# Performance work log

Measured on AMD Instinct MI355X. Metric: run time of the kernel, lower is better.

The kernel has to match this reference:

```python
import jax, jax.numpy as jnp
import numpy as np

N_NODES = 50000
N_EDGES = 800000
N_GRAPHS = 128


def gcn_conv(x, row, col, W, b, num_nodes):
    # GCNConv: x' = D^-1/2 (A + I) D^-1/2 (x W) + b, with self-loops added.
    h = x @ W  # [N, out]
    # append self-loops
    sl = jnp.arange(num_nodes, dtype=row.dtype)
    r = jnp.concatenate([row, sl])
    c = jnp.concatenate([col, sl])
    deg = jax.ops.segment_sum(jnp.ones_like(r, dtype=h.dtype), r, num_segments=num_nodes)
    dinv = jnp.where(deg > 0, jax.lax.rsqrt(deg), 0.0)
    norm = dinv[r] * dinv[c]  # [E+N]
    msg = h[c] * norm[:, None]  # gather + scale
    out = jax.ops.segment_sum(msg, r, num_segments=num_nodes)
    return out + b


def setup_inputs() -> dict:
    key = jax.random.key(0)
    k = jax.random.split(key, 6)
    x = jax.random.normal(k[0], (N_NODES, 256), dtype=jnp.float32)
    edge_index = jax.random.randint(k[1], (2, N_EDGES), 0, N_NODES, dtype=jnp.int32)
    batch = jnp.sort(jax.random.randint(k[2], (N_NODES,), 0, N_GRAPHS, dtype=jnp.int32))
    W1 = jax.random.normal(k[3], (256, 128), dtype=jnp.float32) * (1.0 / np.sqrt(256))
    b1 = jnp.zeros((128,), dtype=jnp.float32)
    W2 = jax.random.normal(k[4], (128, 32), dtype=jnp.float32) * (1.0 / np.sqrt(128))
    b2 = jnp.zeros((32,), dtype=jnp.float32)
    return {"x": x, "edge_index": edge_index, "batch": batch,
            "W1": W1, "b1": b1, "W2": W2, "b2": b2}


def reference(x, edge_index, batch, W1, b1, W2, b2):
    row, col = edge_index[0], edge_index[1]
    h = gcn_conv(x, row, col, W1, b1, N_NODES)
    h = jax.nn.relu(h)
    # dropout is identity in eval mode (training=False)
    h = gcn_conv(h, row, col, W2, b2, N_NODES)
    # global_mean_pool over batch ids
    sums = jax.ops.segment_sum(h, batch, num_segments=N_GRAPHS)
    cnts = jax.ops.segment_sum(jnp.ones((N_NODES,), dtype=h.dtype), batch, num_segments=N_GRAPHS)
    pooled = sums / jnp.clip(cnts, 1.0)[:, None]  # [G, num_classes]
    return jax.nn.log_softmax(pooled, axis=1)
```

## Files before the change

### kernel.cpp

```cpp
#include <hip/hip_runtime.h>
#include <math.h>

#define N_NODES 50000
#define N_EDGES 800000
#define N_GRAPHS 128
#define DIM0 256
#define DIM1 128
#define DIM2 32

#define NBUCK 196
#define NEB 98

using f32x4 = __attribute__((ext_vector_type(4))) float;
using s16x8 = __attribute__((ext_vector_type(8))) short;

__device__ inline unsigned bf16pack(float a, float b) {
    unsigned ua = __float_as_uint(a), ub = __float_as_uint(b);
    ua = (ua + 0x7fffu + ((ua >> 16) & 1u)) >> 16;
    ub = (ub + 0x7fffu + ((ub >> 16) & 1u)) >> 16;
    return ua | (ub << 16);
}
__device__ inline float2 bf16x2(unsigned p) {
    return make_float2(__uint_as_float(p << 16), __uint_as_float(p & 0xffff0000u));
}

__device__ inline int featOf(int p) {
    return 32 * (p >> 5) + ((p >> 1) & 15) + 16 * (p & 1);
}

__global__ __launch_bounds__(256) void k_hist(const int* __restrict__ row, int* __restrict__ hist) {
    __shared__ int h[NBUCK];
    int b = blockIdx.x, t = threadIdx.x;
    if (t < NBUCK) h[t] = 0;
    __syncthreads();
#pragma unroll
    for (int i = 0; i < 8; ++i) {
        int idx = b * 2048 + i * 256 + t;
        if (idx < N_EDGES / 4) {
            int4 r4 = ((const int4*)row)[idx];
            atomicAdd(&h[r4.x >> 8], 1);
            atomicAdd(&h[r4.y >> 8], 1);
            atomicAdd(&h[r4.z >> 8], 1);
            atomicAdd(&h[r4.w >> 8], 1);
        }
    }
    __syncthreads();
    if (t < NBUCK) hist[b * NBUCK + t] = h[t];
}

__global__ __launch_bounds__(256) void k_place(const int* __restrict__ row, const int* __restrict__ col,
                                               const int* __restrict__ hist, uint* __restrict__ bb,
                                               int* __restrict__ bbase, int* __restrict__ btot,
                                               const float* __restrict__ W1, uint* __restrict__ W1b,
                                               const float* __restrict__ W2, uint* __restrict__ W2b,
                                               const int* __restrict__ batch, int* gstart,
                                               float* __restrict__ pooled) {
    __shared__ int cur[NBUCK];
    __shared__ int tot[NBUCK];
    __shared__ int sc[256];
    int blk = blockIdx.x, t = threadIdx.x;
    if (blk >= NEB) {
        if (blk == NEB + 16) {
            for (int i = t; i < N_GRAPHS * DIM2; i += 256) pooled[i] = 0.f;
            return;
        }
        int g = (blk - NEB) * 256 + t;
        {
            int s = g >> 9, tt = (g >> 6) & 7, q = (g >> 4) & 3, n = g & 15;
            int k0 = s * 32 + q * 8;
            int colw = tt * 16 + n;
            uint4 o;
            o.x = bf16pack(W1[(size_t)(k0 + 0) * DIM1 + colw], W1[(size_t)(k0 + 1) * DIM1 + colw]);
            o.y = bf16pack(W1[(size_t)(k0 + 2) * DIM1 + colw], W1[(size_t)(k0 + 3) * DIM1 + colw]);
            o.z = bf16pack(W1[(size_t)(k0 + 4) * DIM1 + colw], W1[(size_t)(k0 + 5) * DIM1 + colw]);
            o.w = bf16pack(W1[(size_t)(k0 + 6) * DIM1 + colw], W1[(size_t)(k0 + 7) * DIM1 + colw]);
            ((uint4*)W1b)[g] = o;
        }
        if (g < 512) {
            int s = g >> 7, tt = (g >> 6) & 1, l = g & 63;
            int n = tt * 16 + (l & 15);
            int kb = s * 32 + (l >> 4) * 8;
            uint4 o;
            o.x = bf16pack(W2[(size_t)featOf(kb + 0) * DIM2 + n], W2[(size_t)featOf(kb + 1) * DIM2 + n]);
            o.y = bf16pack(W2[(size_t)featOf(kb + 2) * DIM2 + n], W2[(size_t)featOf(kb + 3) * DIM2 + n]);
            o.z = bf16pack(W2[(size_t)featOf(kb + 4) * DIM2 + n], W2[(size_t)featOf(kb + 5) * DIM2 + n]);
            o.w = bf16pack(W2[(size_t)featOf(kb + 6) * DIM2 + n], W2[(size_t)featOf(kb + 7) * DIM2 + n]);
            ((uint4*)W2b)[g] = o;
        }
        if (g <= N_GRAPHS) {
            int lo = 0, hi = N_NODES;
            while (lo < hi) { int mid = (lo + hi) >> 1; if (batch[mid] < g) lo = mid + 1; else hi = mid; }
            gstart[g] = lo;
        }
        return;
    }
    int pre = 0, to = 0;
    for (int b2 = 0; b2 < NEB; ++b2) {
        int v = (t < NBUCK) ? hist[b2 * NBUCK + t] : 0;
        to += v;
        if (b2 < blk) pre += v;
    }
    if (t < NBUCK) tot[t] = to;
    sc[t] = (t < NBUCK) ? to : 0;
    __syncthreads();
    for (int off = 1; off < 256; off <<= 1) {
        int x = (t >= off) ? sc[t - off] : 0;
        __syncthreads();
        sc[t] += x;
        __syncthreads();
    }
    if (t < NBUCK) {
        int base = sc[t] - tot[t];
        cur[t] = base + pre;
        if (blk == 0) { bbase[t] = base; btot[t] = tot[t]; }
    }
    __syncthreads();
#pragma unroll
    for (int i = 0; i < 8; ++i) {
        int idx = blk * 2048 + i * 256 + t;
        if (idx < N_EDGES / 4) {
            int4 r4 = ((const int4*)row)[idx];
            int4 c4 = ((const int4*)col)[idx];
            int rs[4] = {r4.x, r4.y, r4.z, r4.w};
            int cs[4] = {c4.x, c4.y, c4.z, c4.w};
#pragma unroll
            for (int j = 0; j < 4; ++j) {
                int pos = atomicAdd(&cur[rs[j] >> 8], 1);
                bb[pos] = ((uint)(rs[j] & 255) << 16) | (uint)cs[j];
            }
        }
    }
}

__global__ __launch_bounds__(256) void k_build(const int* __restrict__ bbase, const int* __restrict__ btot,
                                               const uint* __restrict__ bb,
                                               int* __restrict__ offs, int* __restrict__ cnt,
                                               ushort* __restrict__ csr) {
    __shared__ int c256[256];
    __shared__ int cur256[256];
    __shared__ int wsum[4];
    int b = blockIdx.x, t = threadIdx.x;
    int start = bbase[b];
    int n = btot[b];
    c256[t] = 0;
    __syncthreads();
    for (int i = t; i < n; i += 256) atomicAdd(&c256[bb[start + i] >> 16], 1);
    __syncthreads();
    int w = t >> 6, l = t & 63;
    int v = c256[t];
    int incl = v;
#pragma unroll
    for (int off = 1; off < 64; off <<= 1) {
        int x = __shfl_up(incl, off, 64);
        if (l >= off) incl += x;
    }
    if (l == 63) wsum[w] = incl;
    __syncthreads();
    int woff = 0;
    for (int i = 0; i < w; ++i) woff += wsum[i];
    int excl = incl - v + woff;
    cur256[t] = excl;
    int r = b * 256 + t;
    if (r < N_NODES) { offs[r] = start + excl; cnt[r] = v; }
    __syncthreads();
    for (int i = t; i < n; i += 256) {
        uint e = bb[start + i];
        int pos = atomicAdd(&cur256[e >> 16], 1);
        csr[start + pos] = (ushort)(e & 0xFFFFu);
    }
}

#define G1_BM 128
#define AS_LD 20
__global__ __launch_bounds__(256) void k_gemm1(const float* __restrict__ X, const uint* __restrict__ W1b,
                                               const int* __restrict__ cnt, unsigned* __restrict__ h1u) {
    __shared__ uint w1s[16384];
    __shared__ uint As[G1_BM * AS_LD];
    int t = threadIdx.x;
    int w = t >> 6, lane = t & 63, q = lane >> 4, m16 = lane & 15;
    int rowBase = blockIdx.x * G1_BM;

    {
        const uint4* src = (const uint4*)W1b;
        uint4* dst = (uint4*)w1s;
#pragma unroll
        for (int i = 0; i < 16; ++i) dst[i * 256 + t] = src[i * 256 + t];
    }

    f32x4 acc[2][8];
#pragma unroll
    for (int i = 0; i < 2; ++i)
#pragma unroll
        for (int j = 0; j < 8; ++j) acc[i][j] = (f32x4){0.f, 0.f, 0.f, 0.f};

    int ar = t >> 1, ah = t & 1;
    for (int s = 0; s < 8; ++s) {
        float4 f0 = {0,0,0,0}, f1 = {0,0,0,0}, f2 = {0,0,0,0}, f3 = {0,0,0,0};
        int grow = rowBase + ar;
        if (grow < N_NODES) {
            const float* src = X + (size_t)grow * DIM0 + s * 32 + ah * 16;
            f0 = *(const float4*)(src + 0);
            f1 = *(const float4*)(src + 4);
            f2 = *(const float4*)(src + 8);
            f3 = *(const float4*)(src + 12);
        }
        uint4 p0, p1;
        p0.x = bf16pack(f0.x, f0.y); p0.y = bf16pack(f0.z, f0.w);
        p0.z = bf16pack(f1.x, f1.y); p0.w = bf16pack(f1.z, f1.w);
        p1.x = bf16pack(f2.x, f2.y); p1.y = bf16pack(f2.z, f2.w);
        p1.z = bf16pack(f3.x, f3.y); p1.w = bf16pack(f3.z, f3.w);
        __syncthreads();
        *(uint4*)&As[ar * AS_LD + ah * 8 + 0] = p0;
        *(uint4*)&As[ar * AS_LD + ah * 8 + 4] = p1;
        __syncthreads();

        s16x8 af[2];
#pragma unroll
        for (int rt = 0; rt < 2; ++rt) {
            int arow = w * 32 + rt * 16 + m16;
            af[rt] = *(s16x8*)&As[arow * AS_LD + q * 4];
        }
#pragma unroll
        for (int tt = 0; tt < 8; ++tt) {
            s16x8 bf = *(s16x8*)&w1s[((s * 8 + tt) * 64 + lane) * 4];
            acc[0][tt] = __builtin_amdgcn_mfma_f32_16x16x32_bf16(af[0], bf, acc[0][tt], 0, 0, 0);
            acc[1][tt] = __builtin_amdgcn_mfma_f32_16x16x32_bf16(af[1], bf, acc[1][tt], 0, 0, 0);
        }
    }

#pragma unroll
    for (int rt = 0; rt < 2; ++rt) {
#pragma unroll
        for (int reg = 0; reg < 4; ++reg) {
            int row = rowBase + w * 32 + rt * 16 + q * 4 + reg;
            if (row < N_NODES) {
                float dv = rsqrtf((float)(cnt[row] + 1));
                unsigned* hr = h1u + (size_t)row * 64;
#pragma unroll
                for (int u = 0; u < 4; ++u)
                    hr[u * 16 + m16] = bf16pack(acc[rt][2 * u][reg] * dv, acc[rt][2 * u + 1][reg] * dv);
            }
        }
    }
}

#define A1_LD 68
__global__ __launch_bounds__(256) void k_agg1g2(const unsigned* __restrict__ h1u, const int* __restrict__ cnt,
                                                const int* __restrict__ offs, const ushort* __restrict__ csr,
                                                const float* __restrict__ b1, const uint* __restrict__ W2b,
                                                unsigned* __restrict__ h2u) {
    __shared__ uint a1tile[16 * A1_LD];
    __shared__ float sdi[16];
    int t = threadIdx.x;
    int wv = t >> 6, lane = t & 63;
    int nb16 = blockIdx.x * 16;

#pragma unroll
    for (int i = 0; i < 4; ++i) {
        int m = wv * 4 + i;
        int node = nb16 + m;
        float2 acc = bf16x2(h1u[(size_t)node * 64 + lane]);
        int n = cnt[node];
        const ushort* cp = csr + offs[node];
        int ec = 0;
        if (lane < n) ec = cp[lane];
        int j = 0;
        for (; j + 8 <= n; j += 8) {
            int c0 = __shfl(ec, j),     c1 = __shfl(ec, j + 1), c2 = __shfl(ec, j + 2), c3 = __shfl(ec, j + 3);
            int c4 = __shfl(ec, j + 4), c5 = __shfl(ec, j + 5), c6 = __shfl(ec, j + 6), c7 = __shfl(ec, j + 7);
            unsigned p0 = h1u[(size_t)c0 * 64 + lane];
            unsigned p1 = h1u[(size_t)c1 * 64 + lane];
            unsigned p2 = h1u[(size_t)c2 * 64 + lane];
            unsigned p3 = h1u[(size_t)c3 * 64 + lane];
            unsigned p4 = h1u[(size_t)c4 * 64 + lane];
            unsigned p5 = h1u[(size_t)c5 * 64 + lane];
            unsigned p6 = h1u[(size_t)c6 * 64 + lane];
            unsigned p7 = h1u[(size_t)c7 * 64 + lane];
            float2 v0 = bf16x2(p0), v1 = bf16x2(p1), v2 = bf16x2(p2), v3 = bf16x2(p3);
            float2 v4 = bf16x2(p4), v5 = bf16x2(p5), v6 = bf16x2(p6), v7 = bf16x2(p7);
            acc.x += (v0.x + v1.x) + (v2.x + v3.x) + (v4.x + v5.x) + (v6.x + v7.x);
            acc.y += (v0.y + v1.y) + (v2.y + v3.y) + (v4.y + v5.y) + (v6.y + v7.y);
        }
        for (; j + 4 <= n; j += 4) {
            int c0 = __shfl(ec, j), c1 = __shfl(ec, j + 1), c2 = __shfl(ec, j + 2), c3 = __shfl(ec, j + 3);
            unsigned p0 = h1u[(size_t)c0 * 64 + lane];
            unsigned p1 = h1u[(size_t)c1 * 64 + lane];
            unsigned p2 = h1u[(size_t)c2 * 64 + lane];
            unsigned p3 = h1u[(size_t)c3 * 64 + lane];
            float2 v0 = bf16x2(p0), v1 = bf16x2(p1), v2 = bf16x2(p2), v3 = bf16x2(p3);
            acc.x += (v0.x + v1.x) + (v2.x + v3.x);
            acc.y += (v0.y + v1.y) + (v2.y + v3.y);
        }
        for (; j < n; ++j) {
            int c = __shfl(ec, j);
            float2 v = bf16x2(h1u[(size_t)c * 64 + lane]);
            acc.x += v.x; acc.y += v.y;
        }
        float di = rsqrtf((float)(n + 1));
        if (lane == 0) sdi[m] = di;
        int f0 = (lane >> 4) * 32 + (lane & 15);
        acc.x = fmaxf(acc.x * di + b1[f0], 0.f);
        acc.y = fmaxf(acc.y * di + b1[f0 + 16], 0.f);
        a1tile[m * A1_LD + lane] = bf16pack(acc.x, acc.y);
    }
    __syncthreads();

    if (wv == 0) {
        int q = lane >> 4, m16 = lane & 15;
        f32x4 accA = (f32x4){0.f, 0.f, 0.f, 0.f};
        f32x4 accB = (f32x4){0.f, 0.f, 0.f, 0.f};
#pragma unroll
        for (int s = 0; s < 4; ++s) {
            s16x8 af = *(s16x8*)&a1tile[m16 * A1_LD + s * 16 + q * 4];
            s16x8 bf0 = *(const s16x8*)(W2b + (size_t)((s * 2 + 0) * 64 + lane) * 4);
            s16x8 bf1 = *(const s16x8*)(W2b + (size_t)((s * 2 + 1) * 64 + lane) * 4);
            accA = __builtin_amdgcn_mfma_f32_16x16x32_bf16(af, bf0, accA, 0, 0, 0);
            accB = __builtin_amdgcn_mfma_f32_16x16x32_bf16(af, bf1, accB, 0, 0, 0);
        }
#pragma unroll
        for (int r = 0; r < 4; ++r) {
            int node = nb16 + q * 4 + r;
            float dv = sdi[q * 4 + r];
            h2u[(size_t)node * 16 + m16] = bf16pack(accA[r] * dv, accB[r] * dv);
        }
    }
}

__global__ __launch_bounds__(256) void k_agg2pool(const unsigned* __restrict__ h2u, const int* __restrict__ cnt,
                                                  const int* __restrict__ offs, const ushort* __restrict__ csr,
                                                  const int* __restrict__ batch, float* __restrict__ pooled) {
    __shared__ float2 red[16][16];
    int t = threadIdx.x;
    int nb16 = blockIdx.x * 16;
    int node = nb16 + (t >> 4);
    int l = t & 15;
    float2 acc = bf16x2(h2u[(size_t)node * 16 + l]);
    int n = cnt[node];
    const ushort* cp = csr + offs[node];
    for (int base = 0; base < n; base += 16) {
        int m = min(16, n - base);
        int ec = 0;
        if (l < m) ec = cp[base + l];
        int j = 0;
        for (; j + 4 <= m; j += 4) {
            int c0 = __shfl(ec, j, 16), c1 = __shfl(ec, j + 1, 16);
            int c2 = __shfl(ec, j + 2, 16), c3 = __shfl(ec, j + 3, 16);
            unsigned p0 = h2u[(size_t)c0 * 16 + l];
            unsigned p1 = h2u[(size_t)c1 * 16 + l];
            unsigned p2 = h2u[(size_t)c2 * 16 + l];
            unsigned p3 = h2u[(size_t)c3 * 16 + l];
            float2 v0 = bf16x2(p0), v1 = bf16x2(p1), v2 = bf16x2(p2), v3 = bf16x2(p3);
            acc.x += v0.x + v1.x + v2.x + v3.x;
            acc.y += v0.y + v1.y + v2.y + v3.y;
        }
        for (; j < m; ++j) {
            int c = __shfl(ec, j, 16);
            float2 v = bf16x2(h2u[(size_t)c * 16 + l]);
            acc.x += v.x; acc.y += v.y;
        }
    }
    float di = rsqrtf((float)(n + 1));
    red[t >> 4][l] = make_float2(acc.x * di, acc.y * di);
    __syncthreads();
    if (t < 16) {
        float2 run = make_float2(0.f, 0.f);
        int gprev = batch[nb16];
        for (int m = 0; m < 16; ++m) {
            int g = batch[nb16 + m];
            if (g != gprev) {
                atomicAdd(&pooled[gprev * DIM2 + t], run.x);
                atomicAdd(&pooled[gprev * DIM2 + t + 16], run.y);
                run = make_float2(0.f, 0.f);
                gprev = g;
            }
            float2 v = red[m][t];
            run.x += v.x; run.y += v.y;
        }
        atomicAdd(&pooled[gprev * DIM2 + t], run.x);
        atomicAdd(&pooled[gprev * DIM2 + t + 16], run.y);
    }
}

__global__ __launch_bounds__(64) void k_final(const float* __restrict__ pooled, const int* __restrict__ gstart,
                                              const float* __restrict__ b2, float* __restrict__ out) {
    int g = blockIdx.x;
    int lane = threadIdx.x;
    float cntf = fmaxf((float)(gstart[g + 1] - gstart[g]), 1.0f);
    float val = 0.f, v = -INFINITY;
    if (lane < DIM2) {
        val = pooled[g * DIM2 + lane] / cntf + b2[lane];
        v = val;
    }
#pragma unroll
    for (int m = 16; m >= 1; m >>= 1) v = fmaxf(v, __shfl_xor(v, m, 32));
    float ex = (lane < DIM2) ? expf(val - v) : 0.f;
#pragma unroll
    for (int m = 16; m >= 1; m >>= 1) ex += __shfl_xor(ex, m, 32);
    if (lane < DIM2) out[g * DIM2 + lane] = val - v - logf(ex);
}

extern "C" void kernel_launch(void* const* d_in, const int* in_sizes, int n_in,
                              void* d_out, int out_size, void* d_ws, size_t ws_size,
                              hipStream_t stream) {
    const float* x     = (const float*)d_in[0];
    const int*   eidx  = (const int*)d_in[1];
    const int*   batch = (const int*)d_in[2];
    const float* W1    = (const float*)d_in[3];
    const float* b1    = (const float*)d_in[4];
    const float* W2    = (const float*)d_in[5];
    const float* b2    = (const float*)d_in[6];
    const int* row = eidx;
    const int* col = eidx + N_EDGES;
    float* out = (float*)d_out;

    char* p = (char*)d_ws;
    int*    cnt    = (int*)p;    p += (size_t)N_NODES * 4;
    int*    offs   = (int*)p;    p += (size_t)N_NODES * 4 + 16;
    int*    gstart = (int*)p;    p += 768;
    uint*   W1b    = (uint*)p;   p += 4096 * 16;
    uint*   W2b    = (uint*)p;   p += 512 * 16;
    int*    hist   = (int*)p;    p += (size_t)NEB * NBUCK * 4 + 32;
    int*    bbase  = (int*)p;    p += 1024;
    int*    btot   = (int*)p;    p += 1024;
    float*  pooled = (float*)p;  p += (size_t)N_GRAPHS * DIM2 * 4;
    uint*   bb     = (uint*)p;   p += (size_t)N_EDGES * 4;
    ushort* csr    = (ushort*)p; p += (size_t)N_EDGES * 2;
    unsigned* h1u  = (unsigned*)p; p += (size_t)N_NODES * 64 * 4;
    unsigned* h2u  = (unsigned*)p; p += (size_t)N_NODES * 16 * 4;

    k_hist<<<NEB, 256, 0, stream>>>(row, hist);
    k_place<<<NEB + 17, 256, 0, stream>>>(row, col, hist, bb, bbase, btot,
                                          W1, W1b, W2, W2b, batch, gstart, pooled);
    k_build<<<NBUCK, 256, 0, stream>>>(bbase, btot, bb, offs, cnt, csr);

    k_gemm1<<<(N_NODES + G1_BM - 1) / G1_BM, 256, 0, stream>>>(x, W1b, cnt, h1u);
    k_agg1g2<<<N_NODES / 16, 256, 0, stream>>>(h1u, cnt, offs, csr, b1, W2b, h2u);
    k_agg2pool<<<N_NODES / 16, 256, 0, stream>>>(h2u, cnt, offs, csr, batch, pooled);
    k_final<<<N_GRAPHS, 64, 0, stream>>>(pooled, gstart, b2, out);
}
```

Measured before the change: 191.5 us.

## Fuse CSR construction into one cooperative kernel with global-atomic counting sort

Replaces the three-kernel bucketed CSR build (histogram, bucket placement, per-bucket build) with a single cooperative kernel. It counts per-node degrees with global atomics, runs a grid-wide prefix scan across grid.sync barriers, then scatters column indices with global atomic cursors. This removes two launches and the intermediate bucket buffer. In exchange it relies on contended global atomics on 50k counters, adds five grid-wide barriers, and no longer orders edges deterministically within a row.

```diff
diff --git a/kernel.cpp b/kernel.cpp
--- a/kernel.cpp
+++ b/kernel.cpp
@@ -1,5 +1,8 @@
 #include <hip/hip_runtime.h>
+#include <hip/hip_cooperative_groups.h>
 #include <math.h>
+
+namespace cg = cooperative_groups;
 
 #define N_NODES 50000
 #define N_EDGES 800000
@@ -8,8 +11,7 @@
 #define DIM1 128
 #define DIM2 32
 
-#define NBUCK 196
-#define NEB 98
+#define PRE_GRID 196
 
 using f32x4 = __attribute__((ext_vector_type(4))) float;
 using s16x8 = __attribute__((ext_vector_type(8))) short;
@@ -28,55 +30,46 @@
     return 32 * (p >> 5) + ((p >> 1) & 15) + 16 * (p & 1);
 }
 
-__global__ __launch_bounds__(256) void k_hist(const int* __restrict__ row, int* __restrict__ hist) {
-    __shared__ int h[NBUCK];
+__global__ __launch_bounds__(256) void k_pre(
+    const int* __restrict__ row, const int* __restrict__ col,
+    const float* __restrict__ W1, uint* __restrict__ W1b,
+    const float* __restrict__ W2, uint* __restrict__ W2b,
+    const int* __restrict__ batch, int* __restrict__ gstart,
+    float* __restrict__ pooled,
+    int* __restrict__ deg, int* __restrict__ offs, int* __restrict__ cur,
+    ushort* __restrict__ csr, int* __restrict__ blockTot)
+{
+    cg::grid_group grid = cg::this_grid();
+    __shared__ int wsum[4];
+    __shared__ int sc[256];
     int b = blockIdx.x, t = threadIdx.x;
-    if (t < NBUCK) h[t] = 0;
-    __syncthreads();
-#pragma unroll
-    for (int i = 0; i < 8; ++i) {
-        int idx = b * 2048 + i * 256 + t;
-        if (idx < N_EDGES / 4) {
-            int4 r4 = ((const int4*)row)[idx];
-            atomicAdd(&h[r4.x >> 8], 1);
-            atomicAdd(&h[r4.y >> 8], 1);
-            atomicAdd(&h[r4.z >> 8], 1);
-            atomicAdd(&h[r4.w >> 8], 1);
-        }
-    }
-    __syncthreads();
-    if (t < NBUCK) hist[b * NBUCK + t] = h[t];
-}
-
-__global__ __launch_bounds__(256) void k_place(const int* __restrict__ row, const int* __restrict__ col,
-                                               const int* __restrict__ hist, uint* __restrict__ bb,
-                                               int* __restrict__ bbase, int* __restrict__ btot,
-                                               const float* __restrict__ W1, uint* __restrict__ W1b,
-                                               const float* __restrict__ W2, uint* __restrict__ W2b,
-                                               const int* __restrict__ batch, int* gstart,
-                                               float* __restrict__ pooled) {
-    __shared__ int cur[NBUCK];
-    __shared__ int tot[NBUCK];
-    __shared__ int sc[256];
-    int blk = blockIdx.x, t = threadIdx.x;
-    if (blk >= NEB) {
-        if (blk == NEB + 16) {
-            for (int i = t; i < N_GRAPHS * DIM2; i += 256) pooled[i] = 0.f;
-            return;
-        }
-        int g = (blk - NEB) * 256 + t;
-        {
-            int s = g >> 9, tt = (g >> 6) & 7, q = (g >> 4) & 3, n = g & 15;
-            int k0 = s * 32 + q * 8;
-            int colw = tt * 16 + n;
-            uint4 o;
-            o.x = bf16pack(W1[(size_t)(k0 + 0) * DIM1 + colw], W1[(size_t)(k0 + 1) * DIM1 + colw]);
-            o.y = bf16pack(W1[(size_t)(k0 + 2) * DIM1 + colw], W1[(size_t)(k0 + 3) * DIM1 + colw]);
-            o.z = bf16pack(W1[(size_t)(k0 + 4) * DIM1 + colw], W1[(size_t)(k0 + 5) * DIM1 + colw]);
-            o.w = bf16pack(W1[(size_t)(k0 + 6) * DIM1 + colw], W1[(size_t)(k0 + 7) * DIM1 + colw]);
-            ((uint4*)W1b)[g] = o;
-        }
-        if (g < 512) {
+    int idx = b * 256 + t;
+
+    if (idx < N_NODES) deg[idx] = 0;
+    if (b < 16) pooled[idx] = 0.f;
+    grid.sync();
+
+    const int nI4 = N_EDGES / 4;
+    for (int i = idx; i < nI4; i += PRE_GRID * 256) {
+        int4 r4 = ((const int4*)row)[i];
+        atomicAdd(&deg[r4.x], 1);
+        atomicAdd(&deg[r4.y], 1);
+        atomicAdd(&deg[r4.z], 1);
+        atomicAdd(&deg[r4.w], 1);
+    }
+    if (b < 16) {
+        int g = idx;
+        int s = g >> 9, tt = (g >> 6) & 7, q = (g >> 4) & 3, n = g & 15;
+        int k0 = s * 32 + q * 8;
+        int colw = tt * 16 + n;
+        uint4 o;
+        o.x = bf16pack(W1[(size_t)(k0 + 0) * DIM1 + colw], W1[(size_t)(k0 + 1) * DIM1 + colw]);
+        o.y = bf16pack(W1[(size_t)(k0 + 2) * DIM1 + colw], W1[(size_t)(k0 + 3) * DIM1 + colw]);
+        o.z = bf16pack(W1[(size_t)(k0 + 4) * DIM1 + colw], W1[(size_t)(k0 + 5) * DIM1 + colw]);
+        o.w = bf16pack(W1[(size_t)(k0 + 6) * DIM1 + colw], W1[(size_t)(k0 + 7) * DIM1 + colw]);
+        ((uint4*)W1b)[g] = o;
+    } else if (b == 16) {
+        for (int g = t; g < 512; g += 256) {
             int s = g >> 7, tt = (g >> 6) & 1, l = g & 63;
             int n = tt * 16 + (l & 15);
             int kb = s * 32 + (l >> 4) * 8;
@@ -87,67 +80,17 @@
             o.w = bf16pack(W2[(size_t)featOf(kb + 6) * DIM2 + n], W2[(size_t)featOf(kb + 7) * DIM2 + n]);
             ((uint4*)W2b)[g] = o;
         }
-        if (g <= N_GRAPHS) {
+    } else if (b == 17) {
+        if (t <= N_GRAPHS) {
             int lo = 0, hi = N_NODES;
-            while (lo < hi) { int mid = (lo + hi) >> 1; if (batch[mid] < g) lo = mid + 1; else hi = mid; }
-            gstart[g] = lo;
-        }
-        return;
-    }
-    int pre = 0, to = 0;
-    for (int b2 = 0; b2 < NEB; ++b2) {
-        int v = (t < NBUCK) ? hist[b2 * NBUCK + t] : 0;
-        to += v;
-        if (b2 < blk) pre += v;
-    }
-    if (t < NBUCK) tot[t] = to;
-    sc[t] = (t < NBUCK) ? to : 0;
-    __syncthreads();
-    for (int off = 1; off < 256; off <<= 1) {
-        int x = (t >= off) ? sc[t - off] : 0;
-        __syncthreads();
-        sc[t] += x;
-        __syncthreads();
-    }
-    if (t < NBUCK) {
-        int base = sc[t] - tot[t];
-        cur[t] = base + pre;
-        if (blk == 0) { bbase[t] = base; btot[t] = tot[t]; }
-    }
-    __syncthreads();
-#pragma unroll
-    for (int i = 0; i < 8; ++i) {
-        int idx = blk * 2048 + i * 256 + t;
-        if (idx < N_EDGES / 4) {
-            int4 r4 = ((const int4*)row)[idx];
-            int4 c4 = ((const int4*)col)[idx];
-            int rs[4] = {r4.x, r4.y, r4.z, r4.w};
-            int cs[4] = {c4.x, c4.y, c4.z, c4.w};
-#pragma unroll
-            for (int j = 0; j < 4; ++j) {
-                int pos = atomicAdd(&cur[rs[j] >> 8], 1);
-                bb[pos] = ((uint)(rs[j] & 255) << 16) | (uint)cs[j];
-            }
-        }
-    }
-}
-
-__global__ __launch_bounds__(256) void k_build(const int* __restrict__ bbase, const int* __restrict__ btot,
-                                               const uint* __restrict__ bb,
-                                               int* __restrict__ offs, int* __restrict__ cnt,
-                                               ushort* __restrict__ csr) {
-    __shared__ int c256[256];
-    __shared__ int cur256[256];
-    __shared__ int wsum[4];
-    int b = blockIdx.x, t = threadIdx.x;
-    int start = bbase[b];
-    int n = btot[b];
-    c256[t] = 0;
-    __syncthreads();
-    for (int i = t; i < n; i += 256) atomicAdd(&c256[bb[start + i] >> 16], 1);
-    __syncthreads();
+            while (lo < hi) { int mid = (lo + hi) >> 1; if (batch[mid] < t) lo = mid + 1; else hi = mid; }
+            gstart[t] = lo;
+        }
+    }
+    grid.sync();
+
+    int v = (idx < N_NODES) ? deg[idx] : 0;
     int w = t >> 6, l = t & 63;
-    int v = c256[t];
     int incl = v;
 #pragma unroll
     for (int off = 1; off < 64; off <<= 1) {
@@ -158,15 +101,39 @@
     __syncthreads();
     int woff = 0;
     for (int i = 0; i < w; ++i) woff += wsum[i];
-    int excl = incl - v + woff;
-    cur256[t] = excl;
-    int r = b * 256 + t;
-    if (r < N_NODES) { offs[r] = start + excl; cnt[r] = v; }
-    __syncthreads();
-    for (int i = t; i < n; i += 256) {
-        uint e = bb[start + i];
-        int pos = atomicAdd(&cur256[e >> 16], 1);
-        csr[start + pos] = (ushort)(e & 0xFFFFu);
+    incl += woff;
+    if (t == 255) blockTot[b] = incl;
+    grid.sync();
+
+    if (b == 0) {
+        int tv = (t < PRE_GRID) ? blockTot[t] : 0;
+        sc[t] = tv;
+        __syncthreads();
+        for (int off = 1; off < 256; off <<= 1) {
+            int x = (t >= off) ? sc[t - off] : 0;
+            __syncthreads();
+            sc[t] += x;
+            __syncthreads();
+        }
+        if (t < PRE_GRID) blockTot[t] = sc[t] - tv;
+    }
+    grid.sync();
+
+    int base = blockTot[b];
+    if (idx < N_NODES) {
+        int e = base + incl - v;
+        offs[idx] = e;
+        cur[idx]  = e;
+    }
+    grid.sync();
+
+    for (int i = idx; i < nI4; i += PRE_GRID * 256) {
+        int4 r4 = ((const int4*)row)[i];
+        int4 c4 = ((const int4*)col)[i];
+        int p0 = atomicAdd(&cur[r4.x], 1); csr[p0] = (ushort)c4.x;
+        int p1 = atomicAdd(&cur[r4.y], 1); csr[p1] = (ushort)c4.y;
+        int p2 = atomicAdd(&cur[r4.z], 1); csr[p2] = (ushort)c4.z;
+        int p3 = atomicAdd(&cur[r4.w], 1); csr[p3] = (ushort)c4.w;
     }
 }
 
@@ -414,24 +381,24 @@
     float* out = (float*)d_out;
 
     char* p = (char*)d_ws;
-    int*    cnt    = (int*)p;    p += (size_t)N_NODES * 4;
-    int*    offs   = (int*)p;    p += (size_t)N_NODES * 4 + 16;
-    int*    gstart = (int*)p;    p += 768;
-    uint*   W1b    = (uint*)p;   p += 4096 * 16;
-    uint*   W2b    = (uint*)p;   p += 512 * 16;
-    int*    hist   = (int*)p;    p += (size_t)NEB * NBUCK * 4 + 32;
-    int*    bbase  = (int*)p;    p += 1024;
-    int*    btot   = (int*)p;    p += 1024;
-    float*  pooled = (float*)p;  p += (size_t)N_GRAPHS * DIM2 * 4;
-    uint*   bb     = (uint*)p;   p += (size_t)N_EDGES * 4;
-    ushort* csr    = (ushort*)p; p += (size_t)N_EDGES * 2;
-    unsigned* h1u  = (unsigned*)p; p += (size_t)N_NODES * 64 * 4;
-    unsigned* h2u  = (unsigned*)p; p += (size_t)N_NODES * 16 * 4;
-
-    k_hist<<<NEB, 256, 0, stream>>>(row, hist);
-    k_place<<<NEB + 17, 256, 0, stream>>>(row, col, hist, bb, bbase, btot,
-                                          W1, W1b, W2, W2b, batch, gstart, pooled);
-    k_build<<<NBUCK, 256, 0, stream>>>(bbase, btot, bb, offs, cnt, csr);
+    int*    cnt      = (int*)p;    p += (size_t)N_NODES * 4;
+    int*    offs     = (int*)p;    p += (size_t)N_NODES * 4 + 16;
+    int*    cur      = (int*)p;    p += (size_t)N_NODES * 4 + 16;
+    int*    gstart   = (int*)p;    p += 768;
+    uint*   W1b      = (uint*)p;   p += 4096 * 16;
+    uint*   W2b      = (uint*)p;   p += 512 * 16;
+    int*    blockTot = (int*)p;    p += 1024;
+    float*  pooled   = (float*)p;  p += (size_t)N_GRAPHS * DIM2 * 4;
+    ushort* csr      = (ushort*)p; p += (size_t)N_EDGES * 2;
+    unsigned* h1u    = (unsigned*)p; p += (size_t)N_NODES * 64 * 4;
+    unsigned* h2u    = (unsigned*)p; p += (size_t)N_NODES * 16 * 4;
+
+    void* preArgs[] = {
+        (void*)&row, (void*)&col, (void*)&W1, (void*)&W1b, (void*)&W2, (void*)&W2b,
+        (void*)&batch, (void*)&gstart, (void*)&pooled,
+        (void*)&cnt, (void*)&offs, (void*)&cur, (void*)&csr, (void*)&blockTot
+    };
+    hipLaunchCooperativeKernel((void*)k_pre, dim3(PRE_GRID), dim3(256), preArgs, 0, stream);
 
     k_gemm1<<<(N_NODES + G1_BM - 1) / G1_BM, 256, 0, stream>>>(x, W1b, cnt, h1u);
     k_agg1g2<<<N_NODES / 16, 256, 0, stream>>>(h1u, cnt, offs, csr, b1, W2b, h2u);
```

Measured after the change: 355.2 us. +85.5%, slower.
